# Performance work log

Measured on AMD Instinct MI355X. Metric: run time of the kernel, lower is better.

The kernel has to match this reference:

```python
import jax, jax.numpy as jnp
import numpy as np

N = 100000


def gcn_conv(x, W, b, src, dst, deg_inv_sqrt, n):
    # PyG GCNConv: h = D^{-1/2} (A + I) D^{-1/2} (x W) + b
    h = x @ W  # [N, out]
    norm = deg_inv_sqrt[src] * deg_inv_sqrt[dst]  # [E+N]
    msgs = h[src] * norm[:, None]  # gathered + scaled messages
    out = jax.ops.segment_sum(msgs, dst, num_segments=n)
    return out + b


def _self_loops_and_norm(edge_index, n):
    src, dst = edge_index[0], edge_index[1]
    loop = jnp.arange(n, dtype=edge_index.dtype)
    src = jnp.concatenate([src, loop])
    dst = jnp.concatenate([dst, loop])
    deg = jax.ops.segment_sum(jnp.ones_like(dst, dtype=jnp.float32), dst, num_segments=n)
    deg_inv_sqrt = jnp.where(deg > 0, jax.lax.rsqrt(jnp.maximum(deg, 1.0)), 0.0)
    return src, dst, deg_inv_sqrt


def setup_inputs() -> dict:
    key = jax.random.key(0)
    k1, k2, k3, k4 = jax.random.split(key, 4)
    nfeat, nhid, nclass = 512, 256, 40
    E = 3200000
    x = jax.random.normal(k1, (N, nfeat), dtype=jnp.float32)
    edge_index = jax.random.randint(k2, (2, E), 0, N, dtype=jnp.int64)
    # Glorot-style init for GCNConv weights, zero bias (PyG default)
    W1 = jax.random.normal(k3, (nfeat, nhid), dtype=jnp.float32) / np.sqrt(nfeat)
    b1 = jnp.zeros((nhid,), dtype=jnp.float32)
    W2 = jax.random.normal(k4, (nhid, nclass), dtype=jnp.float32) / np.sqrt(nhid)
    b2 = jnp.zeros((nclass,), dtype=jnp.float32)
    return {"x": x, "W1": W1, "b1": b1, "W2": W2, "b2": b2, "edge_index": edge_index}


def reference(x, W1, b1, W2, b2, edge_index):
    src, dst, dis = _self_loops_and_norm(edge_index, N)
    h = gcn_conv(x, W1, b1, src, dst, dis, N)
    h = jax.nn.relu(h)
    # dropout(p=0.5) is identity in eval mode
    h = gcn_conv(h, W2, b2, src, dst, dis, N)
    return jax.nn.log_softmax(h, axis=1)
```

## Files before the change

kernel.cpp:

```cpp
#include <hip/hip_runtime.h>
#include <math.h>

#define NFEAT 512
#define NHID  256
#define NCLASS 40
#define NBUCK 782
#define BCAP  5120

typedef __attribute__((ext_vector_type(8))) short short8;
typedef __attribute__((ext_vector_type(4))) float f32x4;


__device__ __forceinline__ float bflo(unsigned u) {
    union { unsigned i; float f; } x; x.i = u << 16; return x.f;
}
__device__ __forceinline__ float bfhi(unsigned u) {
    union { unsigned i; float f; } x; x.i = u & 0xffff0000u; return x.f;
}
__device__ __forceinline__ unsigned short f2bf(float f) {
    union { float f; unsigned i; } x; x.f = f;
    unsigned r = x.i + 0x7fffu + ((x.i >> 16) & 1u);
    return (unsigned short)(r >> 16);
}
__device__ __forceinline__ unsigned pack2(float a, float b) {
    return (unsigned)f2bf(a) | ((unsigned)f2bf(b) << 16);
}


__global__ __launch_bounds__(256) void partcast_k(const float* __restrict__ W1,
                                                  unsigned short* __restrict__ WT,
                                                  const int* __restrict__ ei,
                                                  int* bucketCnt,
                                                  unsigned* __restrict__ binned, int E) {
    __shared__ int hist[NBUCK];
    __shared__ int sbase[NBUCK];
    __shared__ int lofs[NBUCK];
    int bid = blockIdx.x;
    int t = threadIdx.x;
    if (bid < (NFEAT * NHID) / 256) {
        int idx = bid * 256 + t;
        int k = idx >> 8;
        int nn = idx & 255;
        WT[(size_t)nn * NFEAT + k] = f2bf(W1[idx]);
        return;
    }
    int pb = bid - (NFEAT * NHID) / 256;
    for (int b = t; b < NBUCK; b += 256) { hist[b] = 0; lofs[b] = 0; }
    __syncthreads();
    int chunk = (E + 255) / 256;
    int beg = pb * chunk;
    int end = beg + chunk; if (end > E) end = E;
    for (int e = beg + t; e < end; e += 256) {
        int d = __builtin_nontemporal_load(ei + (size_t)E + e);
        atomicAdd(&hist[d >> 7], 1);
    }
    __syncthreads();
    for (int b = t; b < NBUCK; b += 256) {
        int h = hist[b];
        if (h) sbase[b] = atomicAdd(&bucketCnt[b], h);
    }
    __syncthreads();
    for (int e = beg + t; e < end; e += 256) {
        int s = __builtin_nontemporal_load(ei + e);
        int d = __builtin_nontemporal_load(ei + (size_t)E + e);
        int b = d >> 7;
        int off = sbase[b] + atomicAdd(&lofs[b], 1);
        __builtin_nontemporal_store(((unsigned)s << 7) | (unsigned)(d & 127),
                                    binned + (size_t)b * BCAP + off);
    }
}


__global__ __launch_bounds__(1024) void bscan_k(const int* __restrict__ bucketCnt,
                                                int* __restrict__ bbase,
                                                int* __restrict__ offs, int n, int E) {
    __shared__ int sd[1024];
    int t = threadIdx.x;
    int v = (t < NBUCK) ? bucketCnt[t] : 0;
    sd[t] = v;
    __syncthreads();
    for (int off = 1; off < 1024; off <<= 1) {
        int add = (t >= off) ? sd[t - off] : 0;
        __syncthreads();
        sd[t] += add;
        __syncthreads();
    }
    if (t < NBUCK) bbase[t] = sd[t] - v;
    if (t == 0) offs[n] = E;
}


__global__ __launch_bounds__(512) void fill2_k(const unsigned* __restrict__ binned,
                                               const int* __restrict__ bucketCnt,
                                               const int* __restrict__ bbase,
                                               int* __restrict__ offs,
                                               float* __restrict__ dis,
                                               int* __restrict__ csrs, int n) {
    __shared__ int h128[128];
    __shared__ int sd[128];
    __shared__ int lcur[128];
    int b = blockIdx.x;
    int t = threadIdx.x;
    int node0 = b << 7;
    int cbt = bucketCnt[b];
    size_t base_in = (size_t)b * BCAP;
    int gbase = bbase[b];
    if (t < 128) h128[t] = 0;
    __syncthreads();
    for (int e = t; e < cbt; e += 512) {
        unsigned u = binned[base_in + e];
        atomicAdd(&h128[u & 127], 1);
    }
    __syncthreads();
    int v = (t < 128) ? h128[t] : 0;
    if (t < 128) sd[t] = v;
    __syncthreads();
    for (int off = 1; off < 128; off <<= 1) {
        int add = (t < 128 && t >= off) ? sd[t - off] : 0;
        __syncthreads();
        if (t < 128) sd[t] += add;
        __syncthreads();
    }
    if (t < 128) {
        int excl = sd[t] - v;
        int nd = node0 + t;
        if (nd < n) {
            offs[nd] = gbase + excl;
            dis[nd] = rsqrtf((float)v + 1.0f);
        }
        lcur[t] = gbase + excl;
    }
    __syncthreads();
    for (int e = t; e < cbt; e += 512) {
        unsigned u = binned[base_in + e];
        int pos = atomicAdd(&lcur[u & 127], 1);
        csrs[pos] = (int)(u >> 7);
    }
}


__global__ __launch_bounds__(256) void gemm1_k(const float* __restrict__ X,
                                               const unsigned short* __restrict__ WT,
                                               const float* __restrict__ dis,
                                               unsigned short* __restrict__ H, int M) {
    __shared__ unsigned short as[64][72];
    __shared__ unsigned short bs[256][72];
    int t = threadIdx.x;
    int lane = t & 63;
    int w = t >> 6;
    int m0 = blockIdx.x * 64;
    int quad = lane >> 4;
    int r16 = lane & 15;

    f32x4 acc[4][4];
#pragma unroll
    for (int a = 0; a < 4; ++a)
#pragma unroll
        for (int b = 0; b < 4; ++b) acc[a][b] = (f32x4){0.f, 0.f, 0.f, 0.f};

    for (int k0 = 0; k0 < NFEAT; k0 += 64) {
        {
            int m = t >> 2;
            int c = (t & 3) * 16;
            int gi = m0 + m;
            float4 v0, v1, v2, v3;
            if (gi < M) {
                const float4* p = (const float4*)(X + (size_t)gi * NFEAT + k0 + c);
                v0 = p[0]; v1 = p[1]; v2 = p[2]; v3 = p[3];
            } else {
                v0 = v1 = v2 = v3 = make_float4(0.f, 0.f, 0.f, 0.f);
            }
            uint4 p0, p1;
            p0.x = pack2(v0.x, v0.y); p0.y = pack2(v0.z, v0.w);
            p0.z = pack2(v1.x, v1.y); p0.w = pack2(v1.z, v1.w);
            p1.x = pack2(v2.x, v2.y); p1.y = pack2(v2.z, v2.w);
            p1.z = pack2(v3.x, v3.y); p1.w = pack2(v3.z, v3.w);
            *(uint4*)&as[m][c] = p0;
            *(uint4*)&as[m][c + 8] = p1;
        }
        {
            const uint4* p = (const uint4*)(WT + (size_t)t * NFEAT + k0);
#pragma unroll
            for (int c = 0; c < 8; ++c) {
                uint4 q = p[c];
                *(uint4*)&bs[t][c * 8] = q;
            }
        }
        __syncthreads();
#pragma unroll
        for (int ks = 0; ks < 64; ks += 32) {
            short8 af[4], bfr[4];
#pragma unroll
            for (int sm = 0; sm < 4; ++sm)
                af[sm] = *(const short8*)&as[sm * 16 + r16][ks + quad * 8];
#pragma unroll
            for (int sn = 0; sn < 4; ++sn)
                bfr[sn] = *(const short8*)&bs[w * 64 + sn * 16 + r16][ks + quad * 8];
#pragma unroll
            for (int sm = 0; sm < 4; ++sm)
#pragma unroll
                for (int sn = 0; sn < 4; ++sn)
                    acc[sm][sn] = __builtin_amdgcn_mfma_f32_16x16x32_bf16(
                        af[sm], bfr[sn], acc[sm][sn], 0, 0, 0);
        }
        __syncthreads();
    }
#pragma unroll
    for (int sm = 0; sm < 4; ++sm) {
#pragma unroll
        for (int rr = 0; rr < 4; ++rr) {
            int row = m0 + sm * 16 + quad * 4 + rr;
            if (row < M) {
                float dsc = dis[row];
#pragma unroll
                for (int sn = 0; sn < 4; ++sn) {
                    int col = w * 64 + sn * 16 + r16;
                    H[(size_t)row * NHID + col] = f2bf(acc[sm][sn][rr] * dsc);
                }
            }
        }
    }
}


__global__ __launch_bounds__(256) void agg1_k(const unsigned short* __restrict__ Hb,
                                              const int* __restrict__ offs,
                                              const int* __restrict__ csrs,
                                              const float* __restrict__ dis,
                                              const float* __restrict__ b1,
                                              unsigned short* __restrict__ outb, int n) {
    int lane = threadIdx.x & 63;
    int i = blockIdx.x * 4 + (threadIdx.x >> 6);
    if (i >= n) return;
    const uint2* Hv = (const uint2*)Hb;
    float a0 = 0.f, a1 = 0.f, a2 = 0.f, a3 = 0.f;
    int beg = offs[i], end = offs[i + 1];
    int e = beg;
    {
        int c[16]; uint2 g[16];
        for (; e + 16 <= end; e += 16) {
#pragma unroll
            for (int u = 0; u < 16; ++u) c[u] = csrs[e + u];
#pragma unroll
            for (int u = 0; u < 16; ++u) g[u] = Hv[(size_t)c[u] * 64 + lane];
#pragma unroll
            for (int u = 0; u < 16; ++u) {
                a0 += bflo(g[u].x); a1 += bfhi(g[u].x);
                a2 += bflo(g[u].y); a3 += bfhi(g[u].y);
            }
        }
        if (e < end) {
#pragma unroll
            for (int u = 0; u < 16; ++u)
                c[u] = (e + u < end) ? csrs[e + u] : i;
#pragma unroll
            for (int u = 0; u < 16; ++u) g[u] = Hv[(size_t)c[u] * 64 + lane];
#pragma unroll
            for (int u = 0; u < 16; ++u) {
                float sel = (e + u < end) ? 1.f : 0.f;
                a0 = fmaf(sel, bflo(g[u].x), a0); a1 = fmaf(sel, bfhi(g[u].x), a1);
                a2 = fmaf(sel, bflo(g[u].y), a2); a3 = fmaf(sel, bfhi(g[u].y), a3);
            }
        }
    }
    uint2 v = Hv[(size_t)i * 64 + lane];
    a0 += bflo(v.x); a1 += bfhi(v.x);
    a2 += bflo(v.y); a3 += bfhi(v.y);
    float di = dis[i];
    float4 bb = ((const float4*)b1)[lane];
    a0 = fmaxf(fmaf(a0, di, bb.x), 0.f); a1 = fmaxf(fmaf(a1, di, bb.y), 0.f);
    a2 = fmaxf(fmaf(a2, di, bb.z), 0.f); a3 = fmaxf(fmaf(a3, di, bb.w), 0.f);
    uint2 o;
    o.x = pack2(a0, a1);
    o.y = pack2(a2, a3);
    ((uint2*)outb)[(size_t)i * 64 + lane] = o;
}


__global__ __launch_bounds__(256) void gemm2_k(const unsigned short* __restrict__ Ab,
                                               const float* __restrict__ W2,
                                               const float* __restrict__ dis,
                                               unsigned short* __restrict__ H2b, int M) {
    __shared__ float w2t[NCLASS][260];
    int t = threadIdx.x;
    for (int idx = t; idx < NHID * NCLASS; idx += 256) {
        int k = idx / NCLASS;
        int j = idx - k * NCLASS;
        w2t[j][k] = W2[idx];
    }
    __syncthreads();
    int i = blockIdx.x * 32 + (t >> 3);
    if (i >= M) return;
    int j0 = (t & 7) * 5;
    const uint2* arow = (const uint2*)(Ab + (size_t)i * NHID);
    float acc[5] = {0.f, 0.f, 0.f, 0.f, 0.f};
#pragma unroll 4
    for (int c = 0; c < 64; ++c) {
        uint2 v = arow[c];
        float a0 = bflo(v.x), a1 = bfhi(v.x), a2 = bflo(v.y), a3 = bfhi(v.y);
        int k = c * 4;
#pragma unroll
        for (int jj = 0; jj < 5; ++jj) {
            float4 q = *(const float4*)&w2t[j0 + jj][k];
            acc[jj] += a0 * q.x + a1 * q.y + a2 * q.z + a3 * q.w;
        }
    }
    float di = dis[i];
#pragma unroll
    for (int jj = 0; jj < 5; ++jj)
        H2b[(size_t)i * 64 + j0 + jj] = f2bf(acc[jj] * di);
    if ((t & 7) < 3)
        ((uint4*)(H2b + (size_t)i * 64 + 40))[t & 7] = make_uint4(0u, 0u, 0u, 0u);
}


__global__ __launch_bounds__(256) void agg2_k(const unsigned short* __restrict__ H2b,
                                              const int* __restrict__ offs,
                                              const int* __restrict__ csrs,
                                              const float* __restrict__ dis,
                                              const float* __restrict__ b2,
                                              float* __restrict__ out, int n) {
    int lane = threadIdx.x & 63;
    int i = blockIdx.x * 4 + (threadIdx.x >> 6);
    if (i >= n) return;
    const uint2* Hv = (const uint2*)H2b;
    int slot = lane >> 4;
    int r16 = lane & 15;
    float a0 = 0.f, a1 = 0.f, a2 = 0.f, a3 = 0.f;
    int beg = offs[i], end = offs[i + 1];
    int e = beg;
    {
        int c[8]; uint2 g[8];
        for (; e + 32 <= end; e += 32) {
#pragma unroll
            for (int u = 0; u < 8; ++u) c[u] = csrs[e + u * 4 + slot];
#pragma unroll
            for (int u = 0; u < 8; ++u) g[u] = Hv[(size_t)c[u] * 16 + r16];
#pragma unroll
            for (int u = 0; u < 8; ++u) {
                a0 += bflo(g[u].x); a1 += bfhi(g[u].x);
                a2 += bflo(g[u].y); a3 += bfhi(g[u].y);
            }
        }
        if (e < end) {
#pragma unroll
            for (int u = 0; u < 8; ++u) {
                int idx = e + u * 4 + slot;
                c[u] = (idx < end) ? csrs[idx] : i;
            }
#pragma unroll
            for (int u = 0; u < 8; ++u) g[u] = Hv[(size_t)c[u] * 16 + r16];
#pragma unroll
            for (int u = 0; u < 8; ++u) {
                float sel = (e + u * 4 + slot < end) ? 1.f : 0.f;
                a0 = fmaf(sel, bflo(g[u].x), a0); a1 = fmaf(sel, bfhi(g[u].x), a1);
                a2 = fmaf(sel, bflo(g[u].y), a2); a3 = fmaf(sel, bfhi(g[u].y), a3);
            }
        }
    }
    if (slot == 0) {
        uint2 v = Hv[(size_t)i * 16 + r16];
        a0 += bflo(v.x); a1 += bfhi(v.x);
        a2 += bflo(v.y); a3 += bfhi(v.y);
    }
    a0 += __shfl_xor(a0, 16, 64); a0 += __shfl_xor(a0, 32, 64);
    a1 += __shfl_xor(a1, 16, 64); a1 += __shfl_xor(a1, 32, 64);
    a2 += __shfl_xor(a2, 16, 64); a2 += __shfl_xor(a2, 32, 64);
    a3 += __shfl_xor(a3, 16, 64); a3 += __shfl_xor(a3, 32, 64);
    float di = dis[i];
    bool act = (r16 < 10);
    float4 bb = act ? ((const float4*)b2)[r16] : make_float4(0.f, 0.f, 0.f, 0.f);
    a0 = fmaf(a0, di, bb.x); a1 = fmaf(a1, di, bb.y);
    a2 = fmaf(a2, di, bb.z); a3 = fmaf(a3, di, bb.w);
    float m = act ? fmaxf(fmaxf(a0, a1), fmaxf(a2, a3)) : -INFINITY;
#pragma unroll
    for (int off = 8; off > 0; off >>= 1) m = fmaxf(m, __shfl_xor(m, off, 16));
    float s = act ? (expf(a0 - m) + expf(a1 - m) + expf(a2 - m) + expf(a3 - m)) : 0.f;
#pragma unroll
    for (int off = 8; off > 0; off >>= 1) s += __shfl_xor(s, off, 16);
    float ls = m + logf(s);
    if (lane < 10) {
        float4 o = make_float4(a0 - ls, a1 - ls, a2 - ls, a3 - ls);
        ((float4*)(out + (size_t)i * NCLASS))[lane] = o;
    }
}


extern "C" void kernel_launch(void* const* d_in, const int* in_sizes, int n_in,
                              void* d_out, int out_size, void* d_ws, size_t ws_size,
                              hipStream_t stream) {
    const float* x  = (const float*)d_in[0];
    const float* W1 = (const float*)d_in[1];
    const float* b1 = (const float*)d_in[2];
    const float* W2 = (const float*)d_in[3];
    const float* b2 = (const float*)d_in[4];
    const int*   ei = (const int*)d_in[5];

    const int N = in_sizes[0] / NFEAT;
    const int E = in_sizes[5] / 2;

    size_t off = 0;
    auto alloc = [&](size_t bytes) { size_t o = off; off += (bytes + 255) & ~(size_t)255; return o; };
    char* ws = (char*)d_ws;
    int*            offs    = (int*)           (ws + alloc((size_t)(N + 1) * 4));
    float*          dis     = (float*)         (ws + alloc((size_t)N * 4));
    int*            bcnt    = (int*)           (ws + alloc((size_t)NBUCK * 4));
    int*            bbase   = (int*)           (ws + alloc((size_t)NBUCK * 4));
    unsigned*       binned  = (unsigned*)      (ws + alloc((size_t)NBUCK * BCAP * 4));
    int*            csrs    = (int*)           (ws + alloc((size_t)E * 4));
    unsigned short* wT      = (unsigned short*)(ws + alloc((size_t)NFEAT * NHID * 2));
    unsigned short* h1b     = (unsigned short*)(ws + alloc((size_t)N * NHID * 2));
    unsigned short* a1b     = (unsigned short*)(ws + alloc((size_t)N * NHID * 2));
    unsigned short* h2b     = (unsigned short*)(ws + alloc((size_t)N * 64 * 2));
    float*          out     = (float*)d_out;

    hipMemsetAsync(bcnt, 0, (size_t)NBUCK * 4, stream);
    partcast_k<<<(NFEAT * NHID) / 256 + 256, 256, 0, stream>>>(W1, wT, ei, bcnt, binned, E);
    bscan_k<<<1, 1024, 0, stream>>>(bcnt, bbase, offs, N, E);
    fill2_k<<<NBUCK, 512, 0, stream>>>(binned, bcnt, bbase, offs, dis, csrs, N);
    gemm1_k<<<(N + 63) / 64, 256, 0, stream>>>(x, wT, dis, h1b, N);
    agg1_k<<<(N + 3) / 4, 256, 0, stream>>>(h1b, offs, csrs, dis, b1, a1b, N);
    gemm2_k<<<(N + 31) / 32, 256, 0, stream>>>(a1b, W2, dis, h2b, N);
    agg2_k<<<(N + 3) / 4, 256, 0, stream>>>(h2b, offs, csrs, dis, b2, out, N);
}
```

Measured before the change: 812.1 us.

## Split layer-1 aggregation into two feature-half passes for cache locality

The layer-1 neighbour aggregation now runs as two launches, each gathering one half (128 bf16 features) of every neighbour row. The gathered working set per pass is halved (about 25 MB instead of 51 MB), so more of it can stay in L2/MALL during the random gathers. In exchange the CSR indices and offsets are read twice, each gather is 4 bytes per lane instead of 8, and there is an extra kernel launch.

```diff
diff --git a/kernel.cpp b/kernel.cpp
--- a/kernel.cpp
+++ b/kernel.cpp
@@ -223,30 +223,31 @@
 }
 
 
-__global__ __launch_bounds__(256) void agg1_k(const unsigned short* __restrict__ Hb,
-                                              const int* __restrict__ offs,
-                                              const int* __restrict__ csrs,
-                                              const float* __restrict__ dis,
-                                              const float* __restrict__ b1,
-                                              unsigned short* __restrict__ outb, int n) {
+__global__ __launch_bounds__(256) void agg1h_k(const unsigned short* __restrict__ Hb,
+                                               const int* __restrict__ offs,
+                                               const int* __restrict__ csrs,
+                                               const float* __restrict__ dis,
+                                               const float* __restrict__ b1,
+                                               unsigned short* __restrict__ outb,
+                                               int n, int f0u) {
     int lane = threadIdx.x & 63;
     int i = blockIdx.x * 4 + (threadIdx.x >> 6);
     if (i >= n) return;
-    const uint2* Hv = (const uint2*)Hb;
-    float a0 = 0.f, a1 = 0.f, a2 = 0.f, a3 = 0.f;
+    const unsigned* Hv = (const unsigned*)Hb;
+    int col = f0u + lane;
+    float a0 = 0.f, a1 = 0.f;
     int beg = offs[i], end = offs[i + 1];
     int e = beg;
     {
-        int c[16]; uint2 g[16];
+        int c[16]; unsigned g[16];
         for (; e + 16 <= end; e += 16) {
 #pragma unroll
             for (int u = 0; u < 16; ++u) c[u] = csrs[e + u];
 #pragma unroll
-            for (int u = 0; u < 16; ++u) g[u] = Hv[(size_t)c[u] * 64 + lane];
+            for (int u = 0; u < 16; ++u) g[u] = Hv[(size_t)c[u] * 128 + col];
 #pragma unroll
             for (int u = 0; u < 16; ++u) {
-                a0 += bflo(g[u].x); a1 += bfhi(g[u].x);
-                a2 += bflo(g[u].y); a3 += bfhi(g[u].y);
+                a0 += bflo(g[u]); a1 += bfhi(g[u]);
             }
         }
         if (e < end) {
@@ -254,26 +255,21 @@
             for (int u = 0; u < 16; ++u)
                 c[u] = (e + u < end) ? csrs[e + u] : i;
 #pragma unroll
-            for (int u = 0; u < 16; ++u) g[u] = Hv[(size_t)c[u] * 64 + lane];
+            for (int u = 0; u < 16; ++u) g[u] = Hv[(size_t)c[u] * 128 + col];
 #pragma unroll
             for (int u = 0; u < 16; ++u) {
                 float sel = (e + u < end) ? 1.f : 0.f;
-                a0 = fmaf(sel, bflo(g[u].x), a0); a1 = fmaf(sel, bfhi(g[u].x), a1);
-                a2 = fmaf(sel, bflo(g[u].y), a2); a3 = fmaf(sel, bfhi(g[u].y), a3);
-            }
-        }
-    }
-    uint2 v = Hv[(size_t)i * 64 + lane];
-    a0 += bflo(v.x); a1 += bfhi(v.x);
-    a2 += bflo(v.y); a3 += bfhi(v.y);
+                a0 = fmaf(sel, bflo(g[u]), a0); a1 = fmaf(sel, bfhi(g[u]), a1);
+            }
+        }
+    }
+    unsigned v = Hv[(size_t)i * 128 + col];
+    a0 += bflo(v); a1 += bfhi(v);
     float di = dis[i];
-    float4 bb = ((const float4*)b1)[lane];
-    a0 = fmaxf(fmaf(a0, di, bb.x), 0.f); a1 = fmaxf(fmaf(a1, di, bb.y), 0.f);
-    a2 = fmaxf(fmaf(a2, di, bb.z), 0.f); a3 = fmaxf(fmaf(a3, di, bb.w), 0.f);
-    uint2 o;
-    o.x = pack2(a0, a1);
-    o.y = pack2(a2, a3);
-    ((uint2*)outb)[(size_t)i * 64 + lane] = o;
+    float2 bb = ((const float2*)b1)[col];
+    a0 = fmaxf(fmaf(a0, di, bb.x), 0.f);
+    a1 = fmaxf(fmaf(a1, di, bb.y), 0.f);
+    ((unsigned*)outb)[(size_t)i * 128 + col] = pack2(a0, a1);
 }
 
 
@@ -419,7 +415,8 @@
     bscan_k<<<1, 1024, 0, stream>>>(bcnt, bbase, offs, N, E);
     fill2_k<<<NBUCK, 512, 0, stream>>>(binned, bcnt, bbase, offs, dis, csrs, N);
     gemm1_k<<<(N + 63) / 64, 256, 0, stream>>>(x, wT, dis, h1b, N);
-    agg1_k<<<(N + 3) / 4, 256, 0, stream>>>(h1b, offs, csrs, dis, b1, a1b, N);
+    agg1h_k<<<(N + 3) / 4, 256, 0, stream>>>(h1b, offs, csrs, dis, b1, a1b, N, 0);
+    agg1h_k<<<(N + 3) / 4, 256, 0, stream>>>(h1b, offs, csrs, dis, b1, a1b, N, 64);
     gemm2_k<<<(N + 31) / 32, 256, 0, stream>>>(a1b, W2, dis, h2b, N);
     agg2_k<<<(N + 3) / 4, 256, 0, stream>>>(h2b, offs, csrs, dis, b2, out, N);
 }
```

Measured after the change: 801.4 us. Within noise of the previous version (-1.3%).
